# Performance work log

Measured on AMD Instinct MI355X. Metric: run time of the kernel, lower is better.

## Reference

```python
import jax, jax.numpy as jnp
import numpy as np

# EdMIPS quantizer constants for 2-bit
HWGQ_STEP = 0.538      # hwgq_steps[2]
GAUSS_STEP = 0.996     # gaussian_steps[2]
ABIT = 2
WBIT = 2
BN_EPS = 1e-3


def setup_inputs() -> dict:
    key = jax.random.key(0)
    k1, k2 = jax.random.split(key, 2)
    x = jax.random.normal(k1, (32, 128, 56, 56), jnp.float32)
    gamma = jnp.ones((128,), jnp.float32)
    beta = jnp.zeros((128,), jnp.float32)
    weight = jax.random.normal(k2, (128, 128, 3, 3), jnp.float32) * 0.05
    return {"x": x, "gamma": gamma, "beta": beta, "weight": weight}


def _hwgq(x):
    # HWGQ: clamp to [0, step*(2^abit - 1)], then round to uniform levels.
    lvls = float(2 ** ABIT - 1)
    thr = HWGQ_STEP * lvls
    y = jnp.clip(x, 0.0, thr)
    q = jnp.round(y / HWGQ_STEP) * HWGQ_STEP
    # straight-through estimator: forward = q, backward = d/dy (clip mask)
    return y + jax.lax.stop_gradient(q - y)


def _gauss_quantize(w):
    # step scaled by weight std (detached, torch uses .item()); mid-rise quantizer.
    step = GAUSS_STEP * jax.lax.stop_gradient(jnp.std(w))
    lvls = float(2 ** WBIT) / 2.0
    q = (jnp.round(w / step + 0.5) - 0.5) * step
    thr = (lvls - 0.5) * step
    q = jnp.clip(q, -thr, thr)
    # full straight-through: backward = identity
    return w + jax.lax.stop_gradient(q - w)


def reference(x, gamma, beta, weight):
    # BatchNorm2d (training-mode batch stats, biased variance, eps=0.001)
    mean = jnp.mean(x, axis=(0, 2, 3), keepdims=True)
    var = jnp.var(x, axis=(0, 2, 3), keepdims=True)
    xn = (x - mean) * jax.lax.rsqrt(var + BN_EPS)
    xn = xn * gamma[None, :, None, None] + beta[None, :, None, None]
    # quantized activations and weights, then plain conv (bias=False)
    a = _hwgq(xn)
    qw = _gauss_quantize(weight)
    out = jax.lax.conv_general_dilated(
        a, qw,
        window_strides=(1, 1),
        padding=((1, 1), (1, 1)),
        dimension_numbers=("NCHW", "OIHW", "NCHW"),
    )
    return out  # [32, 128, 56, 56]
```

## Files before the change

### kernel.cpp

```cpp
#include <hip/hip_runtime.h>

typedef int i32x4 __attribute__((ext_vector_type(4)));

#define C_IN 128
#define HW 56
#define PIX 3136
#define NPLANE 401408
#define PROWB 7424
#define APAD_NSTRIDE 430592

static __device__ __forceinline__ void gload_lds16(const void* g, void* l) {
  __builtin_amdgcn_global_load_lds((__attribute__((address_space(1))) unsigned int*)g,
                                   (__attribute__((address_space(3))) unsigned int*)l, 16, 0, 0);
}

__global__ __launch_bounds__(256) void stats_k(const float* __restrict__ x,
                                               const float* __restrict__ w,
                                               double* __restrict__ bnpart,
                                               double* __restrict__ wpart) {
  const int b = blockIdx.x, tid = threadIdx.x;
  double s = 0.0, s2 = 0.0;
  if (b < 1024) {
    const int c = b & 127, sl = b >> 7;
    for (int n = sl * 4; n < sl * 4 + 4; ++n) {
      const float4* p = (const float4*)(x + (size_t)(n * C_IN + c) * PIX);
      for (int i = tid; i < PIX / 4; i += 256) {
        float4 v = p[i];
        s  += (double)v.x + (double)v.y + (double)v.z + (double)v.w;
        s2 += (double)v.x * v.x + (double)v.y * v.y + (double)v.z * v.z + (double)v.w * v.w;
      }
    }
  } else {
    const int wb = b - 1024;
    const float4* p = (const float4*)w;
    for (int i = wb * 576 + tid; i < (wb + 1) * 576; i += 256) {
      float4 v = p[i];
      s  += (double)v.x + (double)v.y + (double)v.z + (double)v.w;
      s2 += (double)v.x * v.x + (double)v.y * v.y + (double)v.z * v.z + (double)v.w * v.w;
    }
  }
  __shared__ double red[8];
  const int lane = tid & 63, wv = tid >> 6;
  for (int off = 32; off; off >>= 1) { s += __shfl_down(s, off); s2 += __shfl_down(s2, off); }
  if (lane == 0) { red[wv * 2] = s; red[wv * 2 + 1] = s2; }
  __syncthreads();
  if (tid == 0) {
    double* dst = (b < 1024) ? (bnpart + ((b & 127) * 8 + (b >> 7)) * 2)
                             : (wpart + (b - 1024) * 2);
    dst[0] = red[0] + red[2] + red[4] + red[6];
    dst[1] = red[1] + red[3] + red[5] + red[7];
  }
}

__global__ __launch_bounds__(256) void quant_k(const float* __restrict__ x,
                                               const float* __restrict__ w,
                                               const float* __restrict__ gamma,
                                               const float* __restrict__ beta,
                                               const double* __restrict__ bnpart,
                                               const double* __restrict__ wpart,
                                               signed char* __restrict__ apad,
                                               signed char* __restrict__ wq,
                                               float* __restrict__ stepp) {
  const int tid = threadIdx.x;
  if (blockIdx.y == 32) {
    const int bx = blockIdx.x;
    __shared__ float steps;
    __shared__ __align__(16) signed char wl[3 * 1152];
    if (tid < 64) {
      double s = wpart[tid * 2], s2 = wpart[tid * 2 + 1];
      for (int off = 32; off; off >>= 1) { s += __shfl_down(s, off); s2 += __shfl_down(s2, off); }
      if (tid == 0) {
        const double mean = s / 147456.0;
        const double var = s2 / 147456.0 - mean * mean;
        steps = 0.996f * (float)sqrt(var);
        if (bx == 0) stepp[0] = steps;
      }
    }
    __syncthreads();
    const float step = steps;
    for (int i = tid; i < 3456; i += 256) {
      const int oi = i / 1152, rem = i - oi * 1152;
      const int oc = bx + oi * 58;
      if (oc < 128) {
        const int c = rem / 9, rs = rem - c * 9;
        const float v = w[(size_t)(oc * C_IN + c) * 9 + rs];
        float t = 2.f * rintf(v / step + 0.5f) - 1.f;
        t = fminf(fmaxf(t, -3.f), 3.f);
        wl[oi * 1152 + rs * 128 + c] = (signed char)(int)t;
      }
    }
    __syncthreads();
    for (int i = tid; i < 216; i += 256) {
      const int oi = i / 72, rem = i - oi * 72;
      const int oc = bx + oi * 58;
      if (oc < 128) {
        const int rs = rem >> 3, c16 = rem & 7;
        *(uint4*)(wq + rs * 16384 + oc * 128 + c16 * 16) =
            *(const uint4*)(wl + oi * 1152 + rs * 128 + c16 * 16);
      }
    }
    return;
  }
  const int hh = blockIdx.x;
  const int n = blockIdx.y;
  __shared__ float2 aff[128];
  __shared__ __align__(16) signed char lds[58 * 144];
  if (tid < 128) {
    double s = 0.0, s2 = 0.0;
    for (int i = 0; i < 8; ++i) { s += bnpart[(tid * 8 + i) * 2]; s2 += bnpart[(tid * 8 + i) * 2 + 1]; }
    const double mean = s / 100352.0;
    const double var = s2 / 100352.0 - mean * mean;
    const double inv = 1.0 / sqrt(var + 1e-3);
    aff[tid] = make_float2((float)((double)gamma[tid] * inv),
                           (float)((double)beta[tid] - mean * inv * (double)gamma[tid]));
  }
  uint4* lds4 = (uint4*)lds;
  for (int i = tid; i < 58 * 144 / 16; i += 256) lds4[i] = make_uint4(0, 0, 0, 0);
  __syncthreads();
  if (hh >= 1 && hh <= 56) {
    const float* xp = x + (size_t)n * NPLANE + (hh - 1) * HW;
    for (int i = tid; i < C_IN * HW; i += 256) {
      const int ww = i % HW, c = i / HW;
      const float v = xp[(size_t)c * PIX + ww];
      const float2 af = aff[c];
      const float xn = fmaf(v, af.x, af.y);
      const float y = fminf(fmaxf(xn, 0.f), 1.614f);
      lds[(ww + 1) * 144 + c] = (signed char)(int)rintf(y * (1.f / 0.538f));
    }
  }
  __syncthreads();
  signed char* dst = apad + (size_t)n * APAD_NSTRIDE;
  for (int i = tid; i < 58 * 8; i += 256) {
    const int col = i >> 3, c16 = i & 7;
    const int pp = hh * 58 + col;
    *(uint4*)(dst + (((size_t)pp * 128 + c16 * 16) ^ ((pp & 7) << 4))) = lds4[col * 9 + c16];
  }
}

__global__ __launch_bounds__(256, 2) void conv_k(const signed char* __restrict__ apad,
                                                 const signed char* __restrict__ wq,
                                                 const float* __restrict__ stepp,
                                                 float* __restrict__ out) {
  __shared__ __align__(16) signed char Al[45056];
  const int bid = blockIdx.x;
  const int vid = (bid & 7) * 112 + (bid >> 3);
  const int n = vid / 28;
  const int rem = vid - n * 28;
  const int rg = rem >> 1;
  const int oh = rem & 1;
  const int tid = threadIdx.x;
  const int wv = tid >> 6, lane = tid & 63;
  const int lr = lane & 15, q4 = lane >> 4;
  const int kq = q4 * 16;
  const int ocb = oh * 64 + (wv & 1) * 32;
  const int phalf = (wv >> 1) * 112;

  {
    const signed char* gsrc = apad + (size_t)n * APAD_NSTRIDE + (size_t)(rg * 4) * PROWB;
    for (int i = wv; i < 44; i += 4)
      if (i < 43 || lane < 32)
        gload_lds16(gsrc + i * 1024 + lane * 16, Al + i * 1024);
  }

  i32x4 wreg[9][2][2];
  {
    const signed char* wb = wq + (ocb + lr) * 128 + kq;
#pragma unroll
    for (int rs = 0; rs < 9; ++rs)
#pragma unroll
      for (int k64 = 0; k64 < 2; ++k64)
#pragma unroll
        for (int of = 0; of < 2; ++of)
          wreg[rs][k64][of] = *(const i32x4*)(wb + rs * 16384 + of * 2048 + k64 * 64);
  }

  int pbase[7];
#pragma unroll
  for (int pf = 0; pf < 7; ++pf) {
    const int po = phalf + pf * 16 + lr;
    pbase[pf] = (po / 56) * 58 + po % 56;
  }

  i32x4 acc[7][2];
#pragma unroll
  for (int i = 0; i < 7; ++i) {
    acc[i][0] = (i32x4){0, 0, 0, 0};
    acc[i][1] = (i32x4){0, 0, 0, 0};
  }

  __syncthreads();

#pragma unroll
  for (int rs = 0; rs < 9; ++rs) {
    const int poff = (rs / 3) * 58 + (rs % 3);
#pragma unroll
    for (int k64 = 0; k64 < 2; ++k64) {
      const int kb = k64 * 64 + kq;
#pragma unroll
      for (int pf = 0; pf < 7; ++pf) {
        const int pp = pbase[pf] + poff;
        const i32x4 bf = *(const i32x4*)(Al + ((pp * 128 + kb) ^ ((pp & 7) << 4)));
        acc[pf][0] = __builtin_amdgcn_mfma_i32_16x16x64_i8(wreg[rs][k64][0], bf, acc[pf][0], 0, 0, 0);
        acc[pf][1] = __builtin_amdgcn_mfma_i32_16x16x64_i8(wreg[rs][k64][1], bf, acc[pf][1], 0, 0, 0);
      }
    }
  }

  const float oscale = 0.269f * stepp[0];
  float* outn = out + (size_t)n * NPLANE + (size_t)rg * 224;
#pragma unroll
  for (int pf = 0; pf < 7; ++pf) {
    const int po = phalf + pf * 16 + lr;
    float* op = outn + po;
#pragma unroll
    for (int of = 0; of < 2; ++of) {
      const int oc = ocb + of * 16 + q4 * 4;
#pragma unroll
      for (int q = 0; q < 4; ++q)
        op[(size_t)(oc + q) * PIX] = (float)acc[pf][of][q] * oscale;
    }
  }
}

extern "C" void kernel_launch(void* const* d_in, const int* in_sizes, int n_in,
                              void* d_out, int out_size, void* d_ws, size_t ws_size,
                              hipStream_t stream) {
  const float* x = (const float*)d_in[0];
  const float* gamma = (const float*)d_in[1];
  const float* beta = (const float*)d_in[2];
  const float* w = (const float*)d_in[3];
  float* out = (float*)d_out;
  char* ws = (char*)d_ws;

  double* bnpart = (double*)(ws);
  double* wpart = (double*)(ws + 16384);
  float* stepp = (float*)(ws + 17408);
  signed char* wq = (signed char*)(ws + 18432);
  signed char* apad = (signed char*)(ws + 196608);

  stats_k<<<1088, 256, 0, stream>>>(x, w, bnpart, wpart);
  quant_k<<<dim3(58, 33), 256, 0, stream>>>(x, w, gamma, beta, bnpart, wpart, apad, wq, stepp);
  conv_k<<<896, 256, 0, stream>>>(apad, wq, stepp, out);
}
```

Baseline: 60.69 us.

## Stage conv weights through triple-buffered LDS and retile blocks to two output rows

Each conv block now covers all 128 output channels for two output rows instead of 64 channels for four rows. Weights are no longer held in registers for all nine taps. Per-tap weight slices are streamed into a 3-deep LDS ring with async global-to-LDS loads, and waitcnt/barrier steps overlap the next tap's load with the current tap's MFMAs. Weight rows are XOR-swizzled when written so LDS reads avoid bank conflicts. This lowers register pressure and shrinks the activation tile, but it adds nine barriers and extra LDS traffic per block.

```diff
diff --git a/kernel.cpp b/kernel.cpp
--- a/kernel.cpp
+++ b/kernel.cpp
@@ -95,7 +95,7 @@
       const int oc = bx + oi * 58;
       if (oc < 128) {
         const int rs = rem >> 3, c16 = rem & 7;
-        *(uint4*)(wq + rs * 16384 + oc * 128 + c16 * 16) =
+        *(uint4*)(wq + rs * 16384 + ((oc * 128 + c16 * 16) ^ ((oc & 7) << 4))) =
             *(const uint4*)(wl + oi * 1152 + rs * 128 + c16 * 16);
       }
     }
@@ -141,43 +141,36 @@
                                                  const signed char* __restrict__ wq,
                                                  const float* __restrict__ stepp,
                                                  float* __restrict__ out) {
-  __shared__ __align__(16) signed char Al[45056];
+  __shared__ __align__(16) signed char Al[29696];
+  __shared__ __align__(16) signed char Wl[3][16384];
   const int bid = blockIdx.x;
   const int vid = (bid & 7) * 112 + (bid >> 3);
   const int n = vid / 28;
-  const int rem = vid - n * 28;
-  const int rg = rem >> 1;
-  const int oh = rem & 1;
+  const int rg = vid - n * 28;
   const int tid = threadIdx.x;
   const int wv = tid >> 6, lane = tid & 63;
   const int lr = lane & 15, q4 = lane >> 4;
   const int kq = q4 * 16;
-  const int ocb = oh * 64 + (wv & 1) * 32;
-  const int phalf = (wv >> 1) * 112;
+  const int row0 = wv * 32 + lr;
+  const int wswz = (row0 & 7) << 4;
+  const int rgo = (rg & 1) << 2;
 
   {
-    const signed char* gsrc = apad + (size_t)n * APAD_NSTRIDE + (size_t)(rg * 4) * PROWB;
-    for (int i = wv; i < 44; i += 4)
-      if (i < 43 || lane < 32)
-        gload_lds16(gsrc + i * 1024 + lane * 16, Al + i * 1024);
-  }
-
-  i32x4 wreg[9][2][2];
-  {
-    const signed char* wb = wq + (ocb + lr) * 128 + kq;
-#pragma unroll
-    for (int rs = 0; rs < 9; ++rs)
-#pragma unroll
-      for (int k64 = 0; k64 < 2; ++k64)
-#pragma unroll
-        for (int of = 0; of < 2; ++of)
-          wreg[rs][k64][of] = *(const i32x4*)(wb + rs * 16384 + of * 2048 + k64 * 64);
+    const signed char* gsrc = apad + (size_t)n * APAD_NSTRIDE + (size_t)(rg * 2) * PROWB;
+    for (int i = wv; i < 29; i += 4)
+      gload_lds16(gsrc + i * 1024 + lane * 16, Al + i * 1024);
+#pragma unroll
+    for (int i = 0; i < 4; ++i)
+      gload_lds16(wq + (wv + i * 4) * 1024 + lane * 16, &Wl[0][(wv + i * 4) * 1024]);
+#pragma unroll
+    for (int i = 0; i < 4; ++i)
+      gload_lds16(wq + 16384 + (wv + i * 4) * 1024 + lane * 16, &Wl[1][(wv + i * 4) * 1024]);
   }
 
   int pbase[7];
 #pragma unroll
   for (int pf = 0; pf < 7; ++pf) {
-    const int po = phalf + pf * 16 + lr;
+    const int po = pf * 16 + lr;
     pbase[pf] = (po / 56) * 58 + po % 56;
   }
 
@@ -188,33 +181,65 @@
     acc[i][1] = (i32x4){0, 0, 0, 0};
   }
 
-  __syncthreads();
-
-#pragma unroll
-  for (int rs = 0; rs < 9; ++rs) {
-    const int poff = (rs / 3) * 58 + (rs % 3);
-#pragma unroll
-    for (int k64 = 0; k64 < 2; ++k64) {
-      const int kb = k64 * 64 + kq;
-#pragma unroll
-      for (int pf = 0; pf < 7; ++pf) {
-        const int pp = pbase[pf] + poff;
-        const i32x4 bf = *(const i32x4*)(Al + ((pp * 128 + kb) ^ ((pp & 7) << 4)));
-        acc[pf][0] = __builtin_amdgcn_mfma_i32_16x16x64_i8(wreg[rs][k64][0], bf, acc[pf][0], 0, 0, 0);
-        acc[pf][1] = __builtin_amdgcn_mfma_i32_16x16x64_i8(wreg[rs][k64][1], bf, acc[pf][1], 0, 0, 0);
-      }
-    }
-  }
+  asm volatile("s_waitcnt vmcnt(4)" ::: "memory");
+  __builtin_amdgcn_sched_barrier(0);
+  __builtin_amdgcn_s_barrier();
+  __builtin_amdgcn_sched_barrier(0);
+
+#define ISSUE(P)                                                                      \
+  {                                                                                   \
+    const signed char* ws_ = wq + (P) * 16384;                                        \
+    signed char* wd_ = Wl[(P) % 3];                                                   \
+    _Pragma("unroll")                                                                 \
+    for (int i = 0; i < 4; ++i)                                                       \
+      gload_lds16(ws_ + (wv + i * 4) * 1024 + lane * 16, wd_ + (wv + i * 4) * 1024);  \
+  }
+#define COMP(RS)                                                                      \
+  {                                                                                   \
+    const signed char* Wb = Wl[(RS) % 3];                                             \
+    constexpr int poff_ = ((RS) / 3) * 58 + ((RS) % 3);                               \
+    _Pragma("unroll")                                                                 \
+    for (int k64 = 0; k64 < 2; ++k64) {                                               \
+      const int kb = k64 * 64 + kq;                                                   \
+      const i32x4 wf0 = *(const i32x4*)(Wb + row0 * 128 + (kb ^ wswz));               \
+      const i32x4 wf1 = *(const i32x4*)(Wb + (row0 + 16) * 128 + (kb ^ wswz));        \
+      _Pragma("unroll")                                                               \
+      for (int pf = 0; pf < 7; ++pf) {                                                \
+        const int p = pbase[pf] + poff_;                                              \
+        const i32x4 bf = *(const i32x4*)(Al + p * 128 + (kb ^ (((p + rgo) & 7) << 4)));\
+        acc[pf][0] = __builtin_amdgcn_mfma_i32_16x16x64_i8(wf0, bf, acc[pf][0], 0, 0, 0); \
+        acc[pf][1] = __builtin_amdgcn_mfma_i32_16x16x64_i8(wf1, bf, acc[pf][1], 0, 0, 0); \
+      }                                                                               \
+    }                                                                                 \
+  }
+#define WAITBAR(N)                                    \
+  asm volatile("s_waitcnt vmcnt(" #N ")" ::: "memory"); \
+  __builtin_amdgcn_sched_barrier(0);                  \
+  __builtin_amdgcn_s_barrier();                       \
+  __builtin_amdgcn_sched_barrier(0);
+
+  ISSUE(2) COMP(0) WAITBAR(4)
+  ISSUE(3) COMP(1) WAITBAR(4)
+  ISSUE(4) COMP(2) WAITBAR(4)
+  ISSUE(5) COMP(3) WAITBAR(4)
+  ISSUE(6) COMP(4) WAITBAR(4)
+  ISSUE(7) COMP(5) WAITBAR(4)
+  ISSUE(8) COMP(6) WAITBAR(4)
+           COMP(7) WAITBAR(0)
+           COMP(8)
+#undef ISSUE
+#undef COMP
+#undef WAITBAR
 
   const float oscale = 0.269f * stepp[0];
-  float* outn = out + (size_t)n * NPLANE + (size_t)rg * 224;
+  float* outn = out + (size_t)n * NPLANE + (size_t)rg * 112;
 #pragma unroll
   for (int pf = 0; pf < 7; ++pf) {
-    const int po = phalf + pf * 16 + lr;
+    const int po = pf * 16 + lr;
     float* op = outn + po;
 #pragma unroll
     for (int of = 0; of < 2; ++of) {
-      const int oc = ocb + of * 16 + q4 * 4;
+      const int oc = wv * 32 + of * 16 + q4 * 4;
 #pragma unroll
       for (int q = 0; q < 4; ++q)
         op[(size_t)(oc + q) * PIX] = (float)acc[pf][of][q] * oscale;
```

Measured after the change: 54.32 us. -10.5%, faster.
